# Performance work log

Hardware: AMD Instinct MI355X
Metric: run time of the kernel (lower is better)

## Reference

```python
import jax, jax.numpy as jnp
import numpy as np

N, C_IN, C_OUT = 8192, 128, 128
BN_EPS = 1e-5
EDGE_PROB = 0.004  # avg degree ~33


def setup_inputs() -> dict:
    key = jax.random.key(0)
    k1, k2, k3, k4, k5, k6 = jax.random.split(key, 6)
    node_features = jax.random.normal(k1, (N, C_IN), dtype=jnp.float32)
    # binary dense adjacency (rand fill, thresholded to ~avg degree 33)
    adjacency_matrix = (jax.random.uniform(k2, (N, N)) < EDGE_PROB).astype(jnp.float32)
    s = 1.0 / np.sqrt(C_IN)
    W_n = jax.random.uniform(k3, (C_OUT, C_IN), jnp.float32, -s, s)
    b_n = jax.random.uniform(k4, (C_OUT,), jnp.float32, -s, s)
    W_c = jax.random.uniform(k5, (C_OUT, C_IN), jnp.float32, -s, s)
    b_c = jax.random.uniform(k6, (C_OUT,), jnp.float32, -s, s)
    gamma = jnp.ones((C_OUT,), jnp.float32)
    beta = jnp.zeros((C_OUT,), jnp.float32)
    return {"node_features": node_features, "adjacency_matrix": adjacency_matrix,
            "W_n": W_n, "b_n": b_n, "W_c": W_c, "b_c": b_c,
            "gamma": gamma, "beta": beta}


def reference(node_features, adjacency_matrix, W_n, b_n, W_c, b_c, gamma, beta):
    # mean aggregation: degrees from row-sums (as in the torch code), agg = A.T @ X / deg
    deg = adjacency_matrix.sum(axis=1, keepdims=True)          # [N,1]
    deg = jnp.where(deg == 0, jnp.ones_like(deg), deg)
    agg = (adjacency_matrix.T @ node_features) / deg           # [N,C_in]
    h = agg @ W_n.T + b_n + node_features @ W_c.T + b_c        # [N,C_out]
    # BatchNorm1d, training-mode batch stats (biased variance)
    mu = h.mean(axis=0)
    var = ((h - mu) ** 2).mean(axis=0)
    h_norm = (h - mu) * jax.lax.rsqrt(var + BN_EPS)
    return jax.nn.relu(gamma * h_norm + beta)
```

## Files before the change

### kernel.cpp

```cpp
#include <hip/hip_runtime.h>
#include <stdint.h>

#define NN 8192
#define CC 128
#define BN_EPS 1e-5f

__device__ inline unsigned short f2bf(float f) {
    unsigned int u = __float_as_uint(f);
    unsigned int r = (u + 0x7fffu + ((u >> 16) & 1u)) >> 16;
    return (unsigned short)r;
}

__global__ __launch_bounds__(256, 8) void k1a_mask(
        const float* __restrict__ A, unsigned long long* __restrict__ Mt,
        float* __restrict__ deg) {
    __shared__ float dred[4][64];
    const int lane = threadIdx.x & 63;
    const int wave = threadIdx.x >> 6;
    const int task = blockIdx.x * 4 + wave;
    const int band = task >> 6;
    const int i0   = (task & 63) << 7;
    const int j0   = band << 6;

    const uint2* Ap = reinterpret_cast<const uint2*>(A + (size_t)j0 * NN + i0) + lane;
    unsigned long long m0 = 0, m1 = 0;
    float degc = 0.0f;

    #pragma unroll 8
    for (int j = 0; j < 64; ++j) {
        uint2 v = Ap[(size_t)j * (NN / 2)];
        bool n0 = v.x != 0u, n1 = v.y != 0u;
        unsigned long long b0 = __ballot(n0), b1 = __ballot(n1);
        const unsigned long long bit = 1ull << j;
        if (n0) m0 |= bit;
        if (n1) m1 |= bit;
        if (lane == j) degc = (float)(__popcll(b0) + __popcll(b1));
    }

    unsigned long long* p = Mt + (size_t)band * NN + i0 + 2 * lane;
    *reinterpret_cast<ulonglong2*>(p) = make_ulonglong2(m0, m1);

    dred[wave][lane] = degc;
    __syncthreads();
    if (wave == 0) {
        float s = dred[0][lane] + dred[1][lane] + dred[2][lane] + dred[3][lane];
        atomicAdd(&deg[j0 + lane], s);
    }
}

__global__ __launch_bounds__(256, 8) void k1c_gather(
        const unsigned long long* __restrict__ Mt, const float* __restrict__ X,
        const float* __restrict__ deg, float* __restrict__ aggN) {
    __shared__ float red[4][128];
    const int lane = threadIdx.x & 63;
    const int wave = threadIdx.x >> 6;
    const int i = blockIdx.x;

    unsigned long long w = 0;
    if (lane < 32)
        w = Mt[(size_t)(wave * 32 + lane) * NN + i];
    float acc0 = 0.0f, acc1 = 0.0f;

    unsigned long long any = __ballot(w != 0ull);
    while (any) {
        int q = __builtin_ctzll(any); any &= any - 1;
        unsigned long long u = __shfl(w, q);
        const float* Xq = X + (size_t)((wave * 32 + q) * 64) * CC;
        while (u) {
            int b = __builtin_ctzll(u); u &= u - 1;
            const float* xr = Xq + b * CC;
            acc0 += xr[lane];
            acc1 += xr[64 + lane];
        }
    }

    red[wave][lane]      = acc0;
    red[wave][64 + lane] = acc1;
    __syncthreads();
    if (wave == 0) {
        float s0 = red[0][lane]      + red[1][lane]      + red[2][lane]      + red[3][lane];
        float s1 = red[0][64 + lane] + red[1][64 + lane] + red[2][64 + lane] + red[3][64 + lane];
        float d  = deg[i];
        float rd = (d == 0.0f) ? 1.0f : (1.0f / d);
        aggN[(size_t)i * CC + lane]      = s0 * rd;
        aggN[(size_t)i * CC + 64 + lane] = s1 * rd;
    }
}

__global__ __launch_bounds__(256, 2) void k2_gemm(
        const float* __restrict__ aggN, const float* __restrict__ X,
        const float* __restrict__ Wn, const float* __restrict__ bn,
        const float* __restrict__ Wc, const float* __restrict__ bc,
        float* __restrict__ h, float* __restrict__ bsum, float* __restrict__ bsq) {
    __shared__ unsigned int Wp[128 * 128];
    const int tid = threadIdx.x;
    for (int idx = tid * 4; idx < 128 * 128; idx += 1024) {
        float4 wn4 = *reinterpret_cast<const float4*>(Wn + idx);
        float4 wc4 = *reinterpret_cast<const float4*>(Wc + idx);
        int c = idx >> 7, k0 = idx & 127;
        #pragma unroll
        for (int q = 0; q < 4; ++q) {
            unsigned int pk = (unsigned int)f2bf((&wn4.x)[q])
                            | ((unsigned int)f2bf((&wc4.x)[q]) << 16);
            int k = k0 + q;
            Wp[(k * 128 + c) ^ (k & 31)] = pk;
        }
    }
    __syncthreads();
    const int c  = tid & 127;
    const int rg = tid >> 7;
    const int i0 = blockIdx.x * 16 + rg * 8;

    float accN[8], accC[8];
    #pragma unroll
    for (int r = 0; r < 8; ++r) { accN[r] = 0.0f; accC[r] = 0.0f; }

    float4 ar[8], xr[8], an[8], xn[8];

#define LOADK(ab_, xb_, k_) do {                                               \
    _Pragma("unroll")                                                          \
    for (int r = 0; r < 8; ++r) {                                              \
        ab_[r] = *reinterpret_cast<const float4*>(&aggN[(size_t)(i0 + r) * CC + (k_)]); \
        xb_[r] = *reinterpret_cast<const float4*>(&X[(size_t)(i0 + r) * CC + (k_)]);    \
    }                                                                          \
} while (0)

#define COMPK(ab_, xb_, k_) do {                                               \
    _Pragma("unroll")                                                          \
    for (int kk = 0; kk < 4; ++kk) {                                           \
        int kq_ = (k_) + kk;                                                   \
        unsigned int pk_ = Wp[(kq_ * 128 + c) ^ (kq_ & 31)];                   \
        float wn_ = __uint_as_float(pk_ << 16);                                \
        float wc_ = __uint_as_float(pk_ & 0xffff0000u);                        \
        _Pragma("unroll")                                                      \
        for (int r = 0; r < 8; ++r) {                                          \
            accN[r] = fmaf((&ab_[r].x)[kk], wn_, accN[r]);                     \
            accC[r] = fmaf((&xb_[r].x)[kk], wc_, accC[r]);                     \
        }                                                                      \
    }                                                                          \
} while (0)

    LOADK(ar, xr, 0);
    for (int k = 0; k < 128; k += 8) {
        LOADK(an, xn, k + 4);
        COMPK(ar, xr, k);
        if (k + 8 < 128) LOADK(ar, xr, k + 8);
        COMPK(an, xn, k + 4);
    }

    const float bnc = bn[c], bcc = bc[c];
    float sp = 0.0f, sq = 0.0f;
    #pragma unroll
    for (int r = 0; r < 8; ++r) {
        float hv = accN[r] + accC[r] + bnc + bcc;
        h[(size_t)(i0 + r) * CC + c] = hv;
        sp += hv; sq += hv * hv;
    }
    __syncthreads();
    float* red = reinterpret_cast<float*>(Wp);
    red[rg * 128 + c]       = sp;
    red[256 + rg * 128 + c] = sq;
    __syncthreads();
    if (rg == 0) {
        atomicAdd(&bsum[c], red[c] + red[128 + c]);
        atomicAdd(&bsq[c],  red[256 + c] + red[384 + c]);
    }
}

__global__ __launch_bounds__(256) void k4_bn(
        const float* __restrict__ h, const float* __restrict__ bsum,
        const float* __restrict__ bsq, const float* __restrict__ gamma,
        const float* __restrict__ beta, float* __restrict__ out) {
    const int idx = (blockIdx.x * 256 + threadIdx.x) * 4;
    const int c0  = idx & 127;
    float4 hv = *reinterpret_cast<const float4*>(h + idx);
    float4 s4 = *reinterpret_cast<const float4*>(bsum + c0);
    float4 q4 = *reinterpret_cast<const float4*>(bsq + c0);
    float4 g4 = *reinterpret_cast<const float4*>(gamma + c0);
    float4 b4 = *reinterpret_cast<const float4*>(beta + c0);
    const float invN = 1.0f / 8192.0f;
    float4 o;
    const float* hp = &hv.x; const float* sp = &s4.x; const float* qp = &q4.x;
    const float* gp = &g4.x; const float* bp = &b4.x; float* op = &o.x;
    #pragma unroll
    for (int jj = 0; jj < 4; ++jj) {
        float mu  = sp[jj] * invN;
        float var = qp[jj] * invN - mu * mu;
        float sc  = gp[jj] * rsqrtf(var + BN_EPS);
        float v   = (hp[jj] - mu) * sc + bp[jj];
        op[jj] = v > 0.0f ? v : 0.0f;
    }
    *reinterpret_cast<float4*>(out + idx) = o;
}

extern "C" void kernel_launch(void* const* d_in, const int* in_sizes, int n_in,
                              void* d_out, int out_size, void* d_ws, size_t ws_size,
                              hipStream_t stream) {
    const float* X     = (const float*)d_in[0];
    const float* A     = (const float*)d_in[1];
    const float* Wn    = (const float*)d_in[2];
    const float* bn    = (const float*)d_in[3];
    const float* Wc    = (const float*)d_in[4];
    const float* bc    = (const float*)d_in[5];
    const float* gamma = (const float*)d_in[6];
    const float* beta  = (const float*)d_in[7];
    float* out = (float*)d_out;

    char* ws = (char*)d_ws;
    float* deg  = (float*)(ws);
    float* bsum = (float*)(ws + 32768);
    float* bsq  = (float*)(ws + 33280);
    float* aggN = (float*)(ws + 65536);
    unsigned long long* Mt = (unsigned long long*)(ws + 4259840);
    float* h    = (float*)(ws + 4259840);

    hipMemsetAsync(d_ws, 0, 33792, stream);

    k1a_mask  <<<2048, 256, 0, stream>>>(A, Mt, deg);
    k1c_gather<<<8192, 256, 0, stream>>>(Mt, X, deg, aggN);
    k2_gemm   <<<512,  256, 0, stream>>>(aggN, X, Wn, bn, Wc, bc, h, bsum, bsq);
    k4_bn     <<<1024, 256, 0, stream>>>(h, bsum, bsq, gamma, beta, out);
}
```

Before: 446.0 us.

## Split adjacency bitmask into row-contiguous pass plus separate ballot transpose

The mask kernel now reads each adjacency row contiguously with 16-byte loads, builds per-row bitmasks with ballots and writes degrees directly, which removes the deg atomics and most of the memset. A new kernel transposes the 64x64 bit blocks with ballots into the column-major mask, and the gather kernel uses a permuted index to match the resulting bit order. The goal is better coalescing on the dominant 256MB adjacency read. The cost is an extra kernel launch and an 8MB intermediate buffer.

```diff
diff --git a/kernel.cpp b/kernel.cpp
--- a/kernel.cpp
+++ b/kernel.cpp
@@ -11,41 +11,54 @@
     return (unsigned short)r;
 }
 
-__global__ __launch_bounds__(256, 8) void k1a_mask(
-        const float* __restrict__ A, unsigned long long* __restrict__ Mt,
+__global__ __launch_bounds__(256, 8) void k1a_rowmask(
+        const float* __restrict__ A, unsigned long long* __restrict__ M,
         float* __restrict__ deg) {
-    __shared__ float dred[4][64];
+    const int lane = threadIdx.x & 63;
+    const int wave = threadIdx.x >> 6;
+    const int j = blockIdx.x * 4 + wave;
+
+    const uint4* Ap = reinterpret_cast<const uint4*>(A + (size_t)j * NN) + lane;
+    unsigned long long m0 = 0, m1 = 0;
+    int degc = 0;
+
+    #pragma unroll 4
+    for (int t = 0; t < 32; ++t) {
+        uint4 v = Ap[t * 64];
+        unsigned long long b0 = __ballot(v.x != 0u);
+        unsigned long long b1 = __ballot(v.y != 0u);
+        unsigned long long b2 = __ballot(v.z != 0u);
+        unsigned long long b3 = __ballot(v.w != 0u);
+        degc += __popcll(b0) + __popcll(b1) + __popcll(b2) + __popcll(b3);
+        if (lane == 2 * t)     { m0 = b0; m1 = b1; }
+        if (lane == 2 * t + 1) { m0 = b2; m1 = b3; }
+    }
+
+    unsigned long long* p = M + (size_t)j * 128 + 2 * lane;
+    *reinterpret_cast<ulonglong2*>(p) = make_ulonglong2(m0, m1);
+    if (lane == 0) deg[j] = (float)degc;
+}
+
+__global__ __launch_bounds__(256, 8) void k1b_transpose(
+        const unsigned long long* __restrict__ M,
+        unsigned long long* __restrict__ Mt) {
     const int lane = threadIdx.x & 63;
     const int wave = threadIdx.x >> 6;
     const int task = blockIdx.x * 4 + wave;
-    const int band = task >> 6;
-    const int i0   = (task & 63) << 7;
-    const int j0   = band << 6;
-
-    const uint2* Ap = reinterpret_cast<const uint2*>(A + (size_t)j0 * NN + i0) + lane;
-    unsigned long long m0 = 0, m1 = 0;
-    float degc = 0.0f;
+    const int J = task >> 7;
+    const int w = task & 127;
+
+    unsigned long long W = M[(size_t)(J * 64 + lane) * 128 + w];
+    unsigned int Wlo = (unsigned int)W, Whi = (unsigned int)(W >> 32);
+    unsigned long long keep = 0;
 
     #pragma unroll 8
-    for (int j = 0; j < 64; ++j) {
-        uint2 v = Ap[(size_t)j * (NN / 2)];
-        bool n0 = v.x != 0u, n1 = v.y != 0u;
-        unsigned long long b0 = __ballot(n0), b1 = __ballot(n1);
-        const unsigned long long bit = 1ull << j;
-        if (n0) m0 |= bit;
-        if (n1) m1 |= bit;
-        if (lane == j) degc = (float)(__popcll(b0) + __popcll(b1));
-    }
-
-    unsigned long long* p = Mt + (size_t)band * NN + i0 + 2 * lane;
-    *reinterpret_cast<ulonglong2*>(p) = make_ulonglong2(m0, m1);
-
-    dred[wave][lane] = degc;
-    __syncthreads();
-    if (wave == 0) {
-        float s = dred[0][lane] + dred[1][lane] + dred[2][lane] + dred[3][lane];
-        atomicAdd(&deg[j0 + lane], s);
-    }
+    for (int l = 0; l < 64; ++l) {
+        unsigned int bit = (l < 32) ? ((Wlo >> l) & 1u) : ((Whi >> (l - 32)) & 1u);
+        unsigned long long tw = __ballot(bit != 0u);
+        if (lane == l) keep = tw;
+    }
+    Mt[(size_t)J * NN + w * 64 + lane] = keep;
 }
 
 __global__ __launch_bounds__(256, 8) void k1c_gather(
@@ -55,10 +68,11 @@
     const int lane = threadIdx.x & 63;
     const int wave = threadIdx.x >> 6;
     const int i = blockIdx.x;
+    const int pi = (4 * (i >> 8) + (i & 3)) * 64 + ((i & 255) >> 2);
 
     unsigned long long w = 0;
     if (lane < 32)
-        w = Mt[(size_t)(wave * 32 + lane) * NN + i];
+        w = Mt[(size_t)(wave * 32 + lane) * NN + pi];
     float acc0 = 0.0f, acc1 = 0.0f;
 
     unsigned long long any = __ballot(w != 0ull);
@@ -211,13 +225,15 @@
     float* bsum = (float*)(ws + 32768);
     float* bsq  = (float*)(ws + 33280);
     float* aggN = (float*)(ws + 65536);
-    unsigned long long* Mt = (unsigned long long*)(ws + 4259840);
+    unsigned long long* M  = (unsigned long long*)(ws + 4259840);
+    unsigned long long* Mt = (unsigned long long*)(ws + 12648448);
     float* h    = (float*)(ws + 4259840);
 
-    hipMemsetAsync(d_ws, 0, 33792, stream);
-
-    k1a_mask  <<<2048, 256, 0, stream>>>(A, Mt, deg);
-    k1c_gather<<<8192, 256, 0, stream>>>(Mt, X, deg, aggN);
-    k2_gemm   <<<512,  256, 0, stream>>>(aggN, X, Wn, bn, Wc, bc, h, bsum, bsq);
-    k4_bn     <<<1024, 256, 0, stream>>>(h, bsum, bsq, gamma, beta, out);
-}
+    hipMemsetAsync(ws + 32768, 0, 1024, stream);
+
+    k1a_rowmask  <<<2048, 256, 0, stream>>>(A, M, deg);
+    k1b_transpose<<<4096, 256, 0, stream>>>(M, Mt);
+    k1c_gather   <<<8192, 256, 0, stream>>>(Mt, X, deg, aggN);
+    k2_gemm      <<<512,  256, 0, stream>>>(aggN, X, Wn, bn, Wc, bc, h, bsum, bsq);
+    k4_bn        <<<1024, 256, 0, stream>>>(h, bsum, bsq, gamma, beta, out);
+}
```

After: 466.4 us. +4.6%, slower.

## Load-balance neighbor gather with shared edge list over four nodes per block

Applied to the files above, without the earlier changes.

The gather kernel now handles four output nodes per block. It first expands their adjacency bitmasks into a compact shared-memory edge list using an atomic counter. The edges are then split evenly across the four waves, which accumulate gathered feature rows into shared accumulators with atomic adds, unrolled by four for memory-level parallelism. This removes the per-wave imbalance and serialized bit-scanning of the old one-node-per-block scheme, at the cost of LDS atomics and extra synchronization.

```diff
diff --git a/kernel.cpp b/kernel.cpp
--- a/kernel.cpp
+++ b/kernel.cpp
@@ -51,39 +51,67 @@
 __global__ __launch_bounds__(256, 8) void k1c_gather(
         const unsigned long long* __restrict__ Mt, const float* __restrict__ X,
         const float* __restrict__ deg, float* __restrict__ aggN) {
-    __shared__ float red[4][128];
-    const int lane = threadIdx.x & 63;
-    const int wave = threadIdx.x >> 6;
-    const int i = blockIdx.x;
-
-    unsigned long long w = 0;
-    if (lane < 32)
-        w = Mt[(size_t)(wave * 32 + lane) * NN + i];
-    float acc0 = 0.0f, acc1 = 0.0f;
-
-    unsigned long long any = __ballot(w != 0ull);
-    while (any) {
-        int q = __builtin_ctzll(any); any &= any - 1;
-        unsigned long long u = __shfl(w, q);
-        const float* Xq = X + (size_t)((wave * 32 + q) * 64) * CC;
-        while (u) {
-            int b = __builtin_ctzll(u); u &= u - 1;
-            const float* xr = Xq + b * CC;
-            acc0 += xr[lane];
-            acc1 += xr[64 + lane];
+    __shared__ float acc[4][128];
+    __shared__ int   idx[2048];
+    __shared__ int   cnt;
+    const int tid  = threadIdx.x;
+    const int lane = tid & 63;
+    const int wave = tid >> 6;
+    const int i0   = blockIdx.x * 4;
+
+    if (tid == 0) cnt = 0;
+    {
+        float* a = &acc[0][0];
+        a[tid] = 0.0f; a[256 + tid] = 0.0f;
+    }
+    __syncthreads();
+
+    #pragma unroll
+    for (int s = tid; s < 512; s += 256) {
+        int r = s & 3;
+        int w = s >> 2;
+        unsigned long long m = Mt[(size_t)w * NN + i0 + r];
+        while (m) {
+            int b = __builtin_ctzll(m); m &= m - 1;
+            int e = atomicAdd(&cnt, 1);
+            idx[e] = (r << 13) | (w * 64 + b);
         }
     }
-
-    red[wave][lane]      = acc0;
-    red[wave][64 + lane] = acc1;
-    __syncthreads();
-    if (wave == 0) {
-        float s0 = red[0][lane]      + red[1][lane]      + red[2][lane]      + red[3][lane];
-        float s1 = red[0][64 + lane] + red[1][64 + lane] + red[2][64 + lane] + red[3][64 + lane];
-        float d  = deg[i];
+    __syncthreads();
+    const int n  = cnt;
+    const int t0 = (n * wave) >> 2;
+    const int t1 = (n * (wave + 1)) >> 2;
+
+    int t = t0;
+    for (; t + 4 <= t1; t += 4) {
+        int e0 = idx[t], e1 = idx[t + 1], e2 = idx[t + 2], e3 = idx[t + 3];
+        const float* p0 = X + (size_t)(e0 & 8191) * CC;
+        const float* p1 = X + (size_t)(e1 & 8191) * CC;
+        const float* p2 = X + (size_t)(e2 & 8191) * CC;
+        const float* p3 = X + (size_t)(e3 & 8191) * CC;
+        float v00 = p0[lane], v01 = p0[64 + lane];
+        float v10 = p1[lane], v11 = p1[64 + lane];
+        float v20 = p2[lane], v21 = p2[64 + lane];
+        float v30 = p3[lane], v31 = p3[64 + lane];
+        atomicAdd(&acc[e0 >> 13][lane], v00); atomicAdd(&acc[e0 >> 13][64 + lane], v01);
+        atomicAdd(&acc[e1 >> 13][lane], v10); atomicAdd(&acc[e1 >> 13][64 + lane], v11);
+        atomicAdd(&acc[e2 >> 13][lane], v20); atomicAdd(&acc[e2 >> 13][64 + lane], v21);
+        atomicAdd(&acc[e3 >> 13][lane], v30); atomicAdd(&acc[e3 >> 13][64 + lane], v31);
+    }
+    for (; t < t1; ++t) {
+        int e0 = idx[t];
+        const float* p0 = X + (size_t)(e0 & 8191) * CC;
+        float v00 = p0[lane], v01 = p0[64 + lane];
+        atomicAdd(&acc[e0 >> 13][lane], v00); atomicAdd(&acc[e0 >> 13][64 + lane], v01);
+    }
+    __syncthreads();
+
+    #pragma unroll
+    for (int s = tid; s < 512; s += 256) {
+        int r = s >> 7, c = s & 127;
+        float d  = deg[i0 + r];
         float rd = (d == 0.0f) ? 1.0f : (1.0f / d);
-        aggN[(size_t)i * CC + lane]      = s0 * rd;
-        aggN[(size_t)i * CC + 64 + lane] = s1 * rd;
+        aggN[(size_t)(i0 + r) * CC + c] = acc[r][c] * rd;
     }
 }
 
@@ -217,7 +245,7 @@
     hipMemsetAsync(d_ws, 0, 33792, stream);
 
     k1a_mask  <<<2048, 256, 0, stream>>>(A, Mt, deg);
-    k1c_gather<<<8192, 256, 0, stream>>>(Mt, X, deg, aggN);
+    k1c_gather<<<2048, 256, 0, stream>>>(Mt, X, deg, aggN);
     k2_gemm   <<<512,  256, 0, stream>>>(aggN, X, Wn, bn, Wc, bc, h, bsum, bsq);
     k4_bn     <<<1024, 256, 0, stream>>>(h, bsum, bsq, gamma, beta, out);
 }
```

Measured after the change: 608.6 us. +36.4%, slower.

## Stream adjacency rows with wide coalesced loads and add a separate bit-transpose kernel

Applied to the files above, without the earlier changes.

Replaces the band-strided mask kernel with one that reads each adjacency row contiguously, using 16-byte loads per lane. It ballots the nonzero flags into row-major bitmask words and accumulates degrees with per-chunk atomics. A new kernel transposes the bitmask through LDS and a shuffle-based 64x64 bit transpose into the column layout the gather needs. The gather remaps its block index to undo the interleaved column order the ballots produce. The aim is more efficient streaming of the 256 MB dense matrix, at the cost of an extra launch, an intermediate buffer and many more atomics on the degree array.

```diff
diff --git a/kernel.cpp b/kernel.cpp
--- a/kernel.cpp
+++ b/kernel.cpp
@@ -11,40 +11,73 @@
     return (unsigned short)r;
 }
 
-__global__ __launch_bounds__(256, 8) void k1a_mask(
-        const float* __restrict__ A, unsigned long long* __restrict__ Mt,
+__global__ __launch_bounds__(256, 8) void k1a_stream(
+        const float* __restrict__ A, unsigned long long* __restrict__ M,
         float* __restrict__ deg) {
-    __shared__ float dred[4][64];
     const int lane = threadIdx.x & 63;
-    const int wave = threadIdx.x >> 6;
-    const int task = blockIdx.x * 4 + wave;
-    const int band = task >> 6;
-    const int i0   = (task & 63) << 7;
+    const int wid  = (blockIdx.x << 2) + (threadIdx.x >> 6);
+    for (int it = 0; it < 32; ++it) {
+        const int g = wid + (it << 13);
+        const int j = g >> 5;
+        const int t = g & 31;
+        const uint4 v = *(reinterpret_cast<const uint4*>(A + ((size_t)j << 13))
+                          + (t << 6) + lane);
+        unsigned long long b0 = __ballot(v.x != 0u);
+        unsigned long long b1 = __ballot(v.y != 0u);
+        unsigned long long b2 = __ballot(v.z != 0u);
+        unsigned long long b3 = __ballot(v.w != 0u);
+        int cnt = __popcll(b0) + __popcll(b1) + __popcll(b2) + __popcll(b3);
+        unsigned long long w = (lane == 0) ? b0 : (lane == 1) ? b1
+                             : (lane == 2) ? b2 : b3;
+        if (lane < 4)
+            M[(size_t)j * 128 + (t << 2) + lane] = w;
+        if (lane == 0 && cnt)
+            atomicAdd(&deg[j], (float)cnt);
+    }
+}
+
+__global__ __launch_bounds__(256, 8) void k1b_bitT(
+        const unsigned long long* __restrict__ M,
+        unsigned long long* __restrict__ Mt) {
+    __shared__ unsigned long long lds[64 * 33];
+    const int tid  = threadIdx.x;
+    const int lane = tid & 63;
+    const int wave = tid >> 6;
+    const int band = blockIdx.x >> 2;
+    const int W0   = (blockIdx.x & 3) << 5;
     const int j0   = band << 6;
 
-    const uint2* Ap = reinterpret_cast<const uint2*>(A + (size_t)j0 * NN + i0) + lane;
-    unsigned long long m0 = 0, m1 = 0;
-    float degc = 0.0f;
-
-    #pragma unroll 8
-    for (int j = 0; j < 64; ++j) {
-        uint2 v = Ap[(size_t)j * (NN / 2)];
-        bool n0 = v.x != 0u, n1 = v.y != 0u;
-        unsigned long long b0 = __ballot(n0), b1 = __ballot(n1);
-        const unsigned long long bit = 1ull << j;
-        if (n0) m0 |= bit;
-        if (n1) m1 |= bit;
-        if (lane == j) degc = (float)(__popcll(b0) + __popcll(b1));
-    }
-
-    unsigned long long* p = Mt + (size_t)band * NN + i0 + 2 * lane;
-    *reinterpret_cast<ulonglong2*>(p) = make_ulonglong2(m0, m1);
-
-    dred[wave][lane] = degc;
-    __syncthreads();
-    if (wave == 0) {
-        float s = dred[0][lane] + dred[1][lane] + dred[2][lane] + dred[3][lane];
-        atomicAdd(&deg[j0 + lane], s);
+    #pragma unroll
+    for (int e = tid; e < 2048; e += 256) {
+        int jj = e >> 5, ww = e & 31;
+        lds[jj * 33 + ww] = M[(size_t)(j0 + jj) * 128 + W0 + ww];
+    }
+    __syncthreads();
+
+    #pragma unroll
+    for (int s = 0; s < 8; ++s) {
+        const int ww = (wave << 3) + s;
+        unsigned long long x = lds[lane * 33 + ww];
+        #pragma unroll
+        for (int st = 0; st < 6; ++st) {
+            const int jd = 1 << st;
+            const unsigned long long m =
+                (st == 0) ? 0x5555555555555555ull :
+                (st == 1) ? 0x3333333333333333ull :
+                (st == 2) ? 0x0F0F0F0F0F0F0F0Full :
+                (st == 3) ? 0x00FF00FF00FF00FFull :
+                (st == 4) ? 0x0000FFFF0000FFFFull :
+                            0x00000000FFFFFFFFull;
+            unsigned long long p = __shfl_xor(x, jd);
+            if ((lane & jd) == 0) {
+                unsigned long long tt = ((x >> jd) ^ p) & m;
+                x ^= (tt << jd);
+            } else {
+                unsigned long long tt = ((p >> jd) ^ x) & m;
+                x ^= tt;
+            }
+        }
+        Mt[(size_t)band * NN + ((W0 + ww) << 6) + lane] = x;
     }
 }
 
@@ -54,11 +87,13 @@
     __shared__ float red[4][128];
     const int lane = threadIdx.x & 63;
     const int wave = threadIdx.x >> 6;
-    const int i = blockIdx.x;
+    const int v = blockIdx.x;
+    const int W = v >> 6;
+    const int i = ((W >> 2) << 8) + ((v & 63) << 2) + (W & 3);
 
     unsigned long long w = 0;
     if (lane < 32)
-        w = Mt[(size_t)(wave * 32 + lane) * NN + i];
+        w = Mt[(size_t)(wave * 32 + lane) * NN + v];
     float acc0 = 0.0f, acc1 = 0.0f;
 
     unsigned long long any = __ballot(w != 0ull);
@@ -211,12 +246,14 @@
     float* bsum = (float*)(ws + 32768);
     float* bsq  = (float*)(ws + 33280);
     float* aggN = (float*)(ws + 65536);
-    unsigned long long* Mt = (unsigned long long*)(ws + 4259840);
+    unsigned long long* M  = (unsigned long long*)(ws + 4259840);
+    unsigned long long* Mt = (unsigned long long*)(ws + 12648448);
     float* h    = (float*)(ws + 4259840);
 
     hipMemsetAsync(d_ws, 0, 33792, stream);
 
-    k1a_mask  <<<2048, 256, 0, stream>>>(A, Mt, deg);
+    k1a_stream<<<2048, 256, 0, stream>>>(A, M, deg);
+    k1b_bitT  <<<512,  256, 0, stream>>>(M, Mt);
     k1c_gather<<<8192, 256, 0, stream>>>(Mt, X, deg, aggN);
     k2_gemm   <<<512,  256, 0, stream>>>(aggN, X, Wn, bn, Wc, bc, h, bsum, bsq);
     k4_bn     <<<1024, 256, 0, stream>>>(h, bsum, bsq, gamma, beta, out);
```

Measured after the change: 457.8 us. 2.6% more time.
